# Kernel tuning notes

Measured on AMD Instinct MI355X. Metric: run time of the kernel, lower is better.

The kernel has to match this reference:

```python
import jax, jax.numpy as jnp
import numpy as np

B, O, T, C_IN, IMG, P, D = 16, 3, 8, 3, 224, 16, 768
HF = IMG // P  # 14x14 conv feature grid
S = 7          # ObjectsCrops output size (SxS per object per frame)


def setup_inputs() -> dict:
    key = jax.random.key(0)
    ks = jax.random.split(key, 6)
    x = jax.random.normal(ks[0], (B, C_IN, T, IMG, IMG), dtype=jnp.float32)
    # metadata: [B, O, T, 4] boxes (x1,y1,x2,y2) in pixel coords within [0,224]
    u = jax.random.uniform(ks[1], (B, O, T, 4), dtype=jnp.float32)
    bx1 = u[..., 0] * 160.0
    by1 = u[..., 1] * 160.0
    bw = 16.0 + u[..., 2] * 48.0
    bh = 16.0 + u[..., 3] * 48.0
    metadata = jnp.stack([bx1, by1, jnp.minimum(bx1 + bw, 224.0), jnp.minimum(by1 + bh, 224.0)], axis=-1)
    proj_w = jax.random.normal(ks[2], (D, C_IN, P, P), dtype=jnp.float32) * 0.02  # Conv3d kernel, tubelet dim (=1) squeezed
    proj_b = jnp.zeros((D,), dtype=jnp.float32)
    box_categories = jax.random.normal(ks[3], (T, O, D), dtype=jnp.float32) * 0.02
    w1 = jax.random.normal(ks[4], (4, D // 2), dtype=jnp.float32) * 0.1   # Linear(4, 384, bias=False)
    w2 = jax.random.normal(ks[5], (D // 2, D), dtype=jnp.float32) * 0.05  # Linear(384, 768, bias=False)
    return dict(x=x, metadata=metadata, proj_w=proj_w, proj_b=proj_b, box_categories=box_categories, w1=w1, w2=w2)


def _roi_crop(feat, boxes):
    # feat: [BT, C, Hf, Wf]; boxes: [BT, O, 4] (x1,y1,x2,y2) in feature-map coords
    BT, C, Hf, Wf = feat.shape
    x1, y1, x2, y2 = (boxes[..., i] for i in range(4))
    cell = (jnp.arange(S, dtype=feat.dtype) + 0.5) / S               # sample cell centers
    ys = y1[..., None] + cell * (y2 - y1)[..., None]                 # [BT,O,S]
    xs = x1[..., None] + cell * (x2 - x1)[..., None]
    yg = jnp.broadcast_to(ys[:, :, :, None], (BT, O, S, S)) - 0.5    # pixel centers at idx+0.5
    xg = jnp.broadcast_to(xs[:, :, None, :], (BT, O, S, S)) - 0.5
    y0f = jnp.floor(yg); x0f = jnp.floor(xg)
    wy = yg - y0f; wx = xg - x0f
    y0 = jnp.clip(y0f.astype(jnp.int32), 0, Hf - 1); y1i = jnp.clip(y0 + 1, 0, Hf - 1)
    x0 = jnp.clip(x0f.astype(jnp.int32), 0, Wf - 1); x1i = jnp.clip(x0 + 1, 0, Wf - 1)
    gather = jax.vmap(lambda fm, yy, xx: fm[:, yy, xx])              # [C,Hf,Wf],[O,S,S] -> [C,O,S,S]
    v00 = gather(feat, y0, x0); v01 = gather(feat, y0, x1i)
    v10 = gather(feat, y1i, x0); v11 = gather(feat, y1i, x1i)
    wy = wy[:, None]; wx = wx[:, None]                               # [BT,1,O,S,S]
    return (v00 * (1 - wy) * (1 - wx) + v01 * (1 - wy) * wx
            + v10 * wy * (1 - wx) + v11 * wy * wx)                   # [BT,C,O,S,S]


def reference(x, metadata, proj_w, proj_b, box_categories, w1, w2):
    Bs = x.shape[0]
    boxes = jnp.transpose(metadata, (0, 2, 1, 3))                    # [B,T,O,4] pixel coords
    # coordinate MLP on normalized boxes + per-(frame,object) category embedding
    box_emb = jax.nn.relu(jax.nn.relu((boxes / 224.0) @ w1) @ w2)    # [B,T,O,D]
    box_emb = box_categories[None] + box_emb
    # Conv3d patch embed: tubelet=1, stride==kernel -> non-overlapping patchify + GEMM
    xp = x.reshape(Bs, C_IN, T, HF, P, HF, P)
    feat = jnp.einsum('bcthpwq,dcpq->btdhw', xp, proj_w) + proj_b[None, None, :, None, None]
    feat = feat.reshape(Bs * T, D, HF, HF)
    fboxes = boxes.reshape(Bs * T, O, 4) * (HF / 224.0)              # boxes in feature coords
    crops = _roi_crop(feat, fboxes).reshape(Bs, T, D, O, S, S)
    xo = jnp.transpose(crops, (0, 3, 2, 1, 4, 5))                    # [B,O,C,T,S,S]
    emb = jnp.transpose(box_emb, (0, 2, 3, 1))                       # [B,O,D,T]
    xo = xo + emb[..., None, None]
    xo = xo.reshape(Bs * O, D, T, S * S)                             # flatten(3) on [N*O,C,T,H,W]
    return jnp.transpose(xo, (0, 2, 3, 1))                           # [B*O, T, S*S, D]
```

## Files before the change

### kernel.cpp

```cpp
#include <hip/hip_runtime.h>
#include <hip/hip_bf16.h>

typedef unsigned int u32;
typedef unsigned short ushort_t;
typedef __bf16 bf16x8 __attribute__((ext_vector_type(8)));
typedef float f32x4 __attribute__((ext_vector_type(4)));
typedef unsigned short ushort8 __attribute__((ext_vector_type(8)));

#define BB 16
#define OO 3
#define TT 8
#define CIN 3
#define IMG 224
#define PP 16
#define DD 768
#define HFD 14
#define SS 7
#define GM 25088
#define GK 768
#define GN 768

__device__ __forceinline__ ushort_t f2bf(float f) {
    u32 u = __float_as_uint(f);
    u32 r = (u + 0x7FFFu + ((u >> 16) & 1u)) >> 16;
    return (ushort_t)r;
}

__device__ __forceinline__ void load_lds16(const void* g, void* l) {
    __builtin_amdgcn_global_load_lds(
        (const __attribute__((address_space(1))) u32*)g,
        (__attribute__((address_space(3))) u32*)l, 16, 0, 0);
}

__global__ __launch_bounds__(256) void pack_a(const float* __restrict__ x,
                                              ushort_t* __restrict__ Ap) {
    int g = blockIdx.x * 256 + threadIdx.x;
    int m = g / 96;
    int k0 = (g % 96) * 8;
    int w = m % 14;
    int h = (m / 14) % 14;
    int t = (m / 196) % 8;
    int b = m / 1568;
    int c = k0 >> 8;
    int rem = k0 & 255;
    int p = rem >> 4;
    int q0 = rem & 15;
    const float* src = x + ((((size_t)(b * 3 + c) * 8 + t) * 224 + (h * 16 + p)) * 224
                            + (w * 16 + q0));
    f32x4 f0 = *(const f32x4*)src;
    f32x4 f1 = *(const f32x4*)(src + 4);
    ushort8 r;
    r[0] = f2bf(f0[0]); r[1] = f2bf(f0[1]); r[2] = f2bf(f0[2]); r[3] = f2bf(f0[3]);
    r[4] = f2bf(f1[0]); r[5] = f2bf(f1[1]); r[6] = f2bf(f1[2]); r[7] = f2bf(f1[3]);
    *(ushort8*)(Ap + (size_t)m * 768 + k0) = r;
}

__global__ __launch_bounds__(256) void pack_w(const float* __restrict__ w,
                                              ushort_t* __restrict__ Wp) {
    size_t g = ((size_t)blockIdx.x * 256 + threadIdx.x) * 8;
    f32x4 f0 = *(const f32x4*)(w + g);
    f32x4 f1 = *(const f32x4*)(w + g + 4);
    ushort8 r;
    r[0] = f2bf(f0[0]); r[1] = f2bf(f0[1]); r[2] = f2bf(f0[2]); r[3] = f2bf(f0[3]);
    r[4] = f2bf(f1[0]); r[5] = f2bf(f1[1]); r[6] = f2bf(f1[2]); r[7] = f2bf(f1[3]);
    *(ushort8*)(Wp + g) = r;
}

__global__ __launch_bounds__(256) void box_mlp(const float* __restrict__ meta,
                                               const float* __restrict__ w1,
                                               const float* __restrict__ w2,
                                               const float* __restrict__ cats,
                                               float* __restrict__ emb) {
    int bt = blockIdx.x;
    int b = bt / 8, t = bt % 8;
    __shared__ float H[3][384];
    int tid = threadIdx.x;
    for (int idx = tid; idx < 3 * 384; idx += 256) {
        int o = idx / 384, j = idx % 384;
        const float* mp = meta + ((b * 3 + o) * 8 + t) * 4;
        float s = 0.f;
        #pragma unroll
        for (int i = 0; i < 4; ++i) s += (mp[i] * (1.0f / 224.0f)) * w1[i * 384 + j];
        H[o][j] = fmaxf(s, 0.f);
    }
    __syncthreads();
    float acc[3][3] = {};
    for (int j = 0; j < 384; ++j) {
        float w0 = w2[j * 768 + tid];
        float w1v = w2[j * 768 + tid + 256];
        float w2v = w2[j * 768 + tid + 512];
        #pragma unroll
        for (int o = 0; o < 3; ++o) {
            float h = H[o][j];
            acc[o][0] += h * w0;
            acc[o][1] += h * w1v;
            acc[o][2] += h * w2v;
        }
    }
    #pragma unroll
    for (int o = 0; o < 3; ++o)
        #pragma unroll
        for (int c = 0; c < 3; ++c) {
            int d = tid + c * 256;
            emb[((size_t)(b * 8 + t) * 3 + o) * 768 + d] =
                fmaxf(acc[o][c], 0.f) + cats[(t * 3 + o) * 768 + d];
        }
}

__global__ __launch_bounds__(256) void gemm_bt(const ushort_t* __restrict__ A,
                                               const ushort_t* __restrict__ Bt,
                                               const float* __restrict__ pb,
                                               float* __restrict__ C) {
    __shared__ ushort_t lA[128 * 64];
    __shared__ ushort_t lB[128 * 64];
    int tid = threadIdx.x;
    int bm = blockIdx.x % 196;
    int bn = blockIdx.x / 196;
    size_t m0 = (size_t)bm * 128, n0 = (size_t)bn * 128;
    int w = tid >> 6, lane = tid & 63;
    int wr = w >> 1, wc = w & 1;

    f32x4 acc[4][4] = {};

    for (int kt = 0; kt < 12; ++kt) {
        int k0 = kt * 64;
        __syncthreads();
        #pragma unroll
        for (int r = 0; r < 4; ++r) {
            int cidx = r * 256 + tid;
            int row = cidx >> 3;
            int col = (cidx & 7) * 8;
            load_lds16(A + ((m0 + row) * 768 + k0 + col), &lA[(size_t)cidx * 8]);
        }
        #pragma unroll
        for (int r = 0; r < 4; ++r) {
            int cidx = r * 256 + tid;
            int row = cidx >> 3;
            int col = (cidx & 7) * 8;
            load_lds16(Bt + ((n0 + row) * 768 + k0 + col), &lB[(size_t)cidx * 8]);
        }
        __syncthreads();
        #pragma unroll
        for (int kk = 0; kk < 2; ++kk) {
            bf16x8 af[4], bfr[4];
            #pragma unroll
            for (int mi = 0; mi < 4; ++mi)
                af[mi] = *(const bf16x8*)&lA[(wr * 64 + mi * 16 + (lane & 15)) * 64
                                             + kk * 32 + (lane >> 4) * 8];
            #pragma unroll
            for (int ni = 0; ni < 4; ++ni)
                bfr[ni] = *(const bf16x8*)&lB[(wc * 64 + ni * 16 + (lane & 15)) * 64
                                              + kk * 32 + (lane >> 4) * 8];
            #pragma unroll
            for (int mi = 0; mi < 4; ++mi)
                #pragma unroll
                for (int ni = 0; ni < 4; ++ni)
                    acc[mi][ni] = __builtin_amdgcn_mfma_f32_16x16x32_bf16(
                        af[mi], bfr[ni], acc[mi][ni], 0, 0, 0);
        }
    }

    int rbase = (lane >> 4) * 4;
    int cl = lane & 15;
    #pragma unroll
    for (int ni = 0; ni < 4; ++ni) {
        size_t col = n0 + wc * 64 + ni * 16 + cl;
        float pbv = pb[col];
        #pragma unroll
        for (int mi = 0; mi < 4; ++mi) {
            size_t row = m0 + wr * 64 + mi * 16 + rbase;
            #pragma unroll
            for (int j = 0; j < 4; ++j) {
                C[(row + j) * 768 + col] = acc[mi][ni][j] + pbv;
            }
        }
    }
}

__global__ __launch_bounds__(192) void roi_kernel(const float* __restrict__ meta,
                                                  const float* __restrict__ feat,
                                                  const float* __restrict__ emb,
                                                  float* __restrict__ out) {
    int id = blockIdx.x;
    int i = id % 7; id /= 7;
    int o = id % 3; id /= 3;
    int t = id % 8;
    int b = id / 8;

    const float* mp = meta + ((b * 3 + o) * 8 + t) * 4;
    float x1 = mp[0] * (1.f / 16.f);
    float y1 = mp[1] * (1.f / 16.f);
    float x2 = mp[2] * (1.f / 16.f);
    float y2 = mp[3] * (1.f / 16.f);

    float ci = (i + 0.5f) * (1.f / 7.f);
    float yg = y1 + ci * (y2 - y1) - 0.5f;
    float y0f = floorf(yg);
    float wy = yg - y0f;
    int y0 = min(max((int)y0f, 0), 13);
    int y1c = min(y0 + 1, 13);

    int bt = b * 8 + t;
    const float* fbase = feat + (size_t)bt * 196 * 768;
    const float* ep = emb + ((size_t)(b * 8 + t) * 3 + o) * 768;

    int d = threadIdx.x * 4;
    f32x4 ev = *(const f32x4*)(ep + d);

    for (int j = 0; j < 7; ++j) {
        float cj = (j + 0.5f) * (1.f / 7.f);
        float xgv = x1 + cj * (x2 - x1) - 0.5f;
        float x0f = floorf(xgv);
        float wx = xgv - x0f;
        int x0 = min(max((int)x0f, 0), 13);
        int x1i = min(x0 + 1, 13);

        f32x4 v00 = *(const f32x4*)(fbase + ((size_t)y0 * 14 + x0) * 768 + d);
        f32x4 v01 = *(const f32x4*)(fbase + ((size_t)y0 * 14 + x1i) * 768 + d);
        f32x4 v10 = *(const f32x4*)(fbase + ((size_t)y1c * 14 + x0) * 768 + d);
        f32x4 v11 = *(const f32x4*)(fbase + ((size_t)y1c * 14 + x1i) * 768 + d);

        float w00 = (1.f - wy) * (1.f - wx);
        float w01 = (1.f - wy) * wx;
        float w10 = wy * (1.f - wx);
        float w11 = wy * wx;

        f32x4 r;
        #pragma unroll
        for (int e = 0; e < 4; ++e)
            r[e] = v00[e] * w00 + v01[e] * w01 + v10[e] * w10 + v11[e] * w11 + ev[e];

        int pp = i * 7 + j;
        *(f32x4*)(out + ((((size_t)(b * 3 + o) * 8 + t) * 49 + pp) * 768 + d)) = r;
    }
}

extern "C" void kernel_launch(void* const* d_in, const int* in_sizes, int n_in,
                              void* d_out, int out_size, void* d_ws, size_t ws_size,
                              hipStream_t stream) {
    const float* x     = (const float*)d_in[0];
    const float* meta  = (const float*)d_in[1];
    const float* projw = (const float*)d_in[2];
    const float* projb = (const float*)d_in[3];
    const float* cats  = (const float*)d_in[4];
    const float* w1    = (const float*)d_in[5];
    const float* w2    = (const float*)d_in[6];
    float* out = (float*)d_out;

    char* ws = (char*)d_ws;
    const size_t szA   = (size_t)GM * GK * 2;
    const size_t szW   = (size_t)GN * GK * 2;
    const size_t szF   = (size_t)GM * GN * 4;
    ushort_t* Ap  = (ushort_t*)(ws);
    ushort_t* Wp  = (ushort_t*)(ws + szA);
    float*    feat = (float*)(ws + szA + szW);
    float*    emb  = (float*)(ws + szA + szW + szF);

    pack_a<<<9408, 256, 0, stream>>>(x, Ap);
    pack_w<<<288, 256, 0, stream>>>(projw, Wp);
    box_mlp<<<128, 256, 0, stream>>>(meta, w1, w2, cats, emb);
    gemm_bt<<<196 * 6, 256, 0, stream>>>(Ap, Wp, projb, feat);
    roi_kernel<<<16 * 8 * 3 * 7, 192, 0, stream>>>(meta, feat, emb, out);
}
```

Baseline: 273.0 us.

## Fuse patchify and bf16 conversion into GEMM A-tile loading with register prefetch

Removes the separate pack_a kernel and its intermediate bf16 buffer. The GEMM now reads fp32 pixels straight from x, converts them to bf16 in registers and writes them into a padded LDS tile, prefetching the next k-slice during the MFMA work. The box MLP is also split across three blocks per (b,t) to raise parallelism. The cost is that each of the 6 N-blocks re-reads and re-converts the fp32 input instead of reading a packed bf16 copy, and the A loads are now synchronous register loads rather than direct-to-LDS loads.

```diff
diff --git a/kernel.cpp b/kernel.cpp
--- a/kernel.cpp
+++ b/kernel.cpp
@@ -7,18 +7,10 @@
 typedef float f32x4 __attribute__((ext_vector_type(4)));
 typedef unsigned short ushort8 __attribute__((ext_vector_type(8)));
 
-#define BB 16
-#define OO 3
-#define TT 8
-#define CIN 3
-#define IMG 224
-#define PP 16
-#define DD 768
-#define HFD 14
-#define SS 7
 #define GM 25088
 #define GK 768
 #define GN 768
+#define LDA_PAD 72
 
 __device__ __forceinline__ ushort_t f2bf(float f) {
     u32 u = __float_as_uint(f);
@@ -30,29 +22,6 @@
     __builtin_amdgcn_global_load_lds(
         (const __attribute__((address_space(1))) u32*)g,
         (__attribute__((address_space(3))) u32*)l, 16, 0, 0);
-}
-
-__global__ __launch_bounds__(256) void pack_a(const float* __restrict__ x,
-                                              ushort_t* __restrict__ Ap) {
-    int g = blockIdx.x * 256 + threadIdx.x;
-    int m = g / 96;
-    int k0 = (g % 96) * 8;
-    int w = m % 14;
-    int h = (m / 14) % 14;
-    int t = (m / 196) % 8;
-    int b = m / 1568;
-    int c = k0 >> 8;
-    int rem = k0 & 255;
-    int p = rem >> 4;
-    int q0 = rem & 15;
-    const float* src = x + ((((size_t)(b * 3 + c) * 8 + t) * 224 + (h * 16 + p)) * 224
-                            + (w * 16 + q0));
-    f32x4 f0 = *(const f32x4*)src;
-    f32x4 f1 = *(const f32x4*)(src + 4);
-    ushort8 r;
-    r[0] = f2bf(f0[0]); r[1] = f2bf(f0[1]); r[2] = f2bf(f0[2]); r[3] = f2bf(f0[3]);
-    r[4] = f2bf(f1[0]); r[5] = f2bf(f1[1]); r[6] = f2bf(f1[2]); r[7] = f2bf(f1[3]);
-    *(ushort8*)(Ap + (size_t)m * 768 + k0) = r;
 }
 
 __global__ __launch_bounds__(256) void pack_w(const float* __restrict__ w,
@@ -71,7 +40,8 @@
                                                const float* __restrict__ w2,
                                                const float* __restrict__ cats,
                                                float* __restrict__ emb) {
-    int bt = blockIdx.x;
+    int bt = blockIdx.x / 3;
+    int dc = blockIdx.x % 3;
     int b = bt / 8, t = bt % 8;
     __shared__ float H[3][384];
     int tid = threadIdx.x;
@@ -84,34 +54,27 @@
         H[o][j] = fmaxf(s, 0.f);
     }
     __syncthreads();
-    float acc[3][3] = {};
+    int d = dc * 256 + tid;
+    float acc[3] = {0.f, 0.f, 0.f};
+    #pragma unroll 4
     for (int j = 0; j < 384; ++j) {
-        float w0 = w2[j * 768 + tid];
-        float w1v = w2[j * 768 + tid + 256];
-        float w2v = w2[j * 768 + tid + 512];
-        #pragma unroll
-        for (int o = 0; o < 3; ++o) {
-            float h = H[o][j];
-            acc[o][0] += h * w0;
-            acc[o][1] += h * w1v;
-            acc[o][2] += h * w2v;
-        }
+        float wv = w2[j * 768 + d];
+        acc[0] += H[0][j] * wv;
+        acc[1] += H[1][j] * wv;
+        acc[2] += H[2][j] * wv;
     }
     #pragma unroll
-    for (int o = 0; o < 3; ++o)
-        #pragma unroll
-        for (int c = 0; c < 3; ++c) {
-            int d = tid + c * 256;
-            emb[((size_t)(b * 8 + t) * 3 + o) * 768 + d] =
-                fmaxf(acc[o][c], 0.f) + cats[(t * 3 + o) * 768 + d];
-        }
-}
-
-__global__ __launch_bounds__(256) void gemm_bt(const ushort_t* __restrict__ A,
-                                               const ushort_t* __restrict__ Bt,
-                                               const float* __restrict__ pb,
-                                               float* __restrict__ C) {
-    __shared__ ushort_t lA[128 * 64];
+    for (int o = 0; o < 3; ++o) {
+        emb[((size_t)bt * 3 + o) * 768 + d] =
+            fmaxf(acc[o], 0.f) + cats[(t * 3 + o) * 768 + d];
+    }
+}
+
+__global__ __launch_bounds__(256) void gemm_fused(const float* __restrict__ X,
+                                                  const ushort_t* __restrict__ Bt,
+                                                  const float* __restrict__ pb,
+                                                  float* __restrict__ C) {
+    __shared__ ushort_t lA[128 * LDA_PAD];
     __shared__ ushort_t lB[128 * 64];
     int tid = threadIdx.x;
     int bm = blockIdx.x % 196;
@@ -120,18 +83,35 @@
     int w = tid >> 6, lane = tid & 63;
     int wr = w >> 1, wc = w & 1;
 
+    int arow1 = tid >> 2;
+    int arow2 = arow1 + 64;
+    int pseg = tid & 3;
+    int m1 = (int)m0 + arow1;
+    int m2 = m1 + 64;
+    int w1i = m1 % 14, h1 = (m1 / 14) % 14, t1 = (m1 / 196) % 8, b1 = m1 / 1568;
+    int w2i = m2 % 14, h2 = (m2 / 14) % 14, t2 = (m2 / 196) % 8, b2 = m2 / 1568;
+    const float* p1 = X + ((size_t)(b1 * 24 + t1) * 224 + h1 * 16 + pseg) * 224 + w1i * 16;
+    const float* p2 = X + ((size_t)(b2 * 24 + t2) * 224 + h2 * 16 + pseg) * 224 + w2i * 16;
+
+    f32x4 xr0, xr1, xr2, xr3, xr4, xr5, xr6, xr7;
+
+    xr0 = *(const f32x4*)(p1);
+    xr1 = *(const f32x4*)(p1 + 4);
+    xr2 = *(const f32x4*)(p1 + 8);
+    xr3 = *(const f32x4*)(p1 + 12);
+    xr4 = *(const f32x4*)(p2);
+    xr5 = *(const f32x4*)(p2 + 4);
+    xr6 = *(const f32x4*)(p2 + 8);
+    xr7 = *(const f32x4*)(p2 + 12);
+
     f32x4 acc[4][4] = {};
+
+    ushort_t* sA1 = &lA[arow1 * LDA_PAD + pseg * 16];
+    ushort_t* sA2 = &lA[arow2 * LDA_PAD + pseg * 16];
 
     for (int kt = 0; kt < 12; ++kt) {
         int k0 = kt * 64;
         __syncthreads();
-        #pragma unroll
-        for (int r = 0; r < 4; ++r) {
-            int cidx = r * 256 + tid;
-            int row = cidx >> 3;
-            int col = (cidx & 7) * 8;
-            load_lds16(A + ((m0 + row) * 768 + k0 + col), &lA[(size_t)cidx * 8]);
-        }
         #pragma unroll
         for (int r = 0; r < 4; ++r) {
             int cidx = r * 256 + tid;
@@ -139,13 +119,43 @@
             int col = (cidx & 7) * 8;
             load_lds16(Bt + ((n0 + row) * 768 + k0 + col), &lB[(size_t)cidx * 8]);
         }
+        {
+            ushort8 u0, u1;
+            u0[0] = f2bf(xr0[0]); u0[1] = f2bf(xr0[1]); u0[2] = f2bf(xr0[2]); u0[3] = f2bf(xr0[3]);
+            u0[4] = f2bf(xr1[0]); u0[5] = f2bf(xr1[1]); u0[6] = f2bf(xr1[2]); u0[7] = f2bf(xr1[3]);
+            u1[0] = f2bf(xr2[0]); u1[1] = f2bf(xr2[1]); u1[2] = f2bf(xr2[2]); u1[3] = f2bf(xr2[3]);
+            u1[4] = f2bf(xr3[0]); u1[5] = f2bf(xr3[1]); u1[6] = f2bf(xr3[2]); u1[7] = f2bf(xr3[3]);
+            *(ushort8*)(sA1) = u0;
+            *(ushort8*)(sA1 + 8) = u1;
+            ushort8 u2, u3;
+            u2[0] = f2bf(xr4[0]); u2[1] = f2bf(xr4[1]); u2[2] = f2bf(xr4[2]); u2[3] = f2bf(xr4[3]);
+            u2[4] = f2bf(xr5[0]); u2[5] = f2bf(xr5[1]); u2[6] = f2bf(xr5[2]); u2[7] = f2bf(xr5[3]);
+            u3[0] = f2bf(xr6[0]); u3[1] = f2bf(xr6[1]); u3[2] = f2bf(xr6[2]); u3[3] = f2bf(xr6[3]);
+            u3[4] = f2bf(xr7[0]); u3[5] = f2bf(xr7[1]); u3[6] = f2bf(xr7[2]); u3[7] = f2bf(xr7[3]);
+            *(ushort8*)(sA2) = u2;
+            *(ushort8*)(sA2 + 8) = u3;
+        }
         __syncthreads();
+        if (kt < 11) {
+            int ktn = kt + 1;
+            size_t off = (size_t)(ktn >> 2) * 401408 + (size_t)(ktn & 3) * 896;
+            const float* a1 = p1 + off;
+            const float* a2 = p2 + off;
+            xr0 = *(const f32x4*)(a1);
+            xr1 = *(const f32x4*)(a1 + 4);
+            xr2 = *(const f32x4*)(a1 + 8);
+            xr3 = *(const f32x4*)(a1 + 12);
+            xr4 = *(const f32x4*)(a2);
+            xr5 = *(const f32x4*)(a2 + 4);
+            xr6 = *(const f32x4*)(a2 + 8);
+            xr7 = *(const f32x4*)(a2 + 12);
+        }
         #pragma unroll
         for (int kk = 0; kk < 2; ++kk) {
             bf16x8 af[4], bfr[4];
             #pragma unroll
             for (int mi = 0; mi < 4; ++mi)
-                af[mi] = *(const bf16x8*)&lA[(wr * 64 + mi * 16 + (lane & 15)) * 64
+                af[mi] = *(const bf16x8*)&lA[(wr * 64 + mi * 16 + (lane & 15)) * LDA_PAD
                                              + kk * 32 + (lane >> 4) * 8];
             #pragma unroll
             for (int ni = 0; ni < 4; ++ni)
@@ -202,7 +212,7 @@
 
     int bt = b * 8 + t;
     const float* fbase = feat + (size_t)bt * 196 * 768;
-    const float* ep = emb + ((size_t)(b * 8 + t) * 3 + o) * 768;
+    const float* ep = emb + ((size_t)bt * 3 + o) * 768;
 
     int d = threadIdx.x * 4;
     f32x4 ev = *(const f32x4*)(ep + d);
@@ -248,17 +258,14 @@
     float* out = (float*)d_out;
 
     char* ws = (char*)d_ws;
-    const size_t szA   = (size_t)GM * GK * 2;
-    const size_t szW   = (size_t)GN * GK * 2;
-    const size_t szF   = (size_t)GM * GN * 4;
-    ushort_t* Ap  = (ushort_t*)(ws);
-    ushort_t* Wp  = (ushort_t*)(ws + szA);
-    float*    feat = (float*)(ws + szA + szW);
-    float*    emb  = (float*)(ws + szA + szW + szF);
-
-    pack_a<<<9408, 256, 0, stream>>>(x, Ap);
+    const size_t szW = (size_t)GN * GK * 2;
+    const size_t szF = (size_t)GM * GN * 4;
+    ushort_t* Wp   = (ushort_t*)(ws);
+    float*    feat = (float*)(ws + szW);
+    float*    emb  = (float*)(ws + szW + szF);
+
     pack_w<<<288, 256, 0, stream>>>(projw, Wp);
-    box_mlp<<<128, 256, 0, stream>>>(meta, w1, w2, cats, emb);
-    gemm_bt<<<196 * 6, 256, 0, stream>>>(Ap, Wp, projb, feat);
+    box_mlp<<<128 * 3, 256, 0, stream>>>(meta, w1, w2, cats, emb);
+    gemm_fused<<<196 * 6, 256, 0, stream>>>(x, Wp, projb, feat);
     roi_kernel<<<16 * 8 * 3 * 7, 192, 0, stream>>>(meta, feat, emb, out);
 }
```

Result: slower. 295.5 us (+8.3%).
